# Kernel optimization log

Hardware: AMD Instinct MI355X
Metric: run time of the kernel (lower is better)

## Reference

```python
import jax, jax.numpy as jnp
import numpy as np

THRESHOLD = 0.5
J = 3  # dyadic diffusion scales: collect P^t X at t in {1,2,4,8}
COLLECT = (1, 2, 4, 8)


def setup_inputs() -> dict:
    key = jax.random.key(0)
    k1, k2 = jax.random.split(key)
    B, N, d, n_w = 4, 2048, 32, 4
    point_clouds = jax.random.uniform(k1, (B, N, d), dtype=jnp.float32)
    alphas = jax.random.uniform(k2, (n_w, d), dtype=jnp.float32)
    sigma = jnp.asarray(1.0, dtype=jnp.float32)
    return {"point_clouds": point_clouds, "sigma": sigma, "alphas": alphas}


def reference(point_clouds, sigma, alphas):
    # point_clouds: [B, N, d]; alphas: [Wt, d]
    Xb = point_clouds[:, None, :, :] * alphas[None, :, None, :]  # [B,Wt,N,d]
    # pairwise squared distances (compute_dist): diag(G)+diag(G)^T - 2G
    G = jnp.einsum('bwnd,bwmd->bwnm', Xb, Xb)
    sq = jnp.einsum('bwnd,bwnd->bwn', Xb, Xb)
    D = sq[..., :, None] + sq[..., None, :] - 2.0 * G  # [B,Wt,N,N]
    Wm = jnp.exp(-D / sigma)
    Wm = jnp.where(Wm < THRESHOLD, jnp.zeros_like(Wm), Wm)
    # torch W.sum(0) = column sums; W = W / d is column normalization W[i,j]/d[j]
    col = Wm.sum(axis=-2)  # [B,Wt,N]
    Wn = Wm / col[..., None, :]
    N = Xb.shape[2]
    # edge weights are w/2 plus self-loop edges of weight 0.5 -> lazy walk operator
    P = 0.5 * Wn + 0.5 * jnp.eye(N, dtype=Xb.dtype)
    feats = [Xb]
    x = Xb
    for t in range(1, 2 ** J + 1):
        x = jnp.einsum('bwnm,bwmd->bwnd', P, x)
        if t in COLLECT:
            feats.append(x)
    F = jnp.concatenate(feats, axis=-1)  # [B,Wt,N,(len(COLLECT)+1)*d]
    pooled = F.mean(axis=2)  # global mean pool per graph -> [B,Wt,F]
    B = pooled.shape[0]
    return pooled.reshape(B, -1)  # [B, n_weights * F]
```

## Files before the change

### kernel.cpp

```cpp
#include <hip/hip_runtime.h>


#define NPTS   2048
#define DIM    32
#define BATCH  4
#define NW     4
#define NFEAT  5
#define BLK_PER_B 16
#define NBLK   (BATCH * BLK_PER_B)
#define ROWS   (NPTS / BLK_PER_B)
#define OUT_PER_B (NW * NFEAT * DIM)
#define OUT_TOTAL (BATCH * OUT_PER_B)

__global__ __launch_bounds__(256) void partial_sums(const float* __restrict__ pc,
                                                    float* __restrict__ ws) {
    const int b   = blockIdx.x / BLK_PER_B;
    const int blk = blockIdx.x % BLK_PER_B;
    const int t   = threadIdx.x;

    const float4* base = (const float4*)(pc + (size_t)b * NPTS * DIM
                                            + (size_t)blk * ROWS * DIM);
    float4 s = make_float4(0.f, 0.f, 0.f, 0.f);
#pragma unroll
    for (int i = 0; i < 4; ++i) {
        float4 v = base[t + i * 256];
        s.x += v.x; s.y += v.y; s.z += v.z; s.w += v.w;
    }

    __shared__ float4 sm[256];
    sm[t] = s;
    __syncthreads();
#pragma unroll
    for (int str = 128; str >= 8; str >>= 1) {
        if (t < str) {
            float4 a = sm[t], c = sm[t + str];
            a.x += c.x; a.y += c.y; a.z += c.z; a.w += c.w;
            sm[t] = a;
        }
        __syncthreads();
    }
    if (t < DIM)
        ws[blockIdx.x * DIM + t] = ((const float*)sm)[t];
}

__global__ __launch_bounds__(256) void combine(const float* __restrict__ ws,
                                               const float* __restrict__ alphas,
                                               float* __restrict__ out) {
    const int t = threadIdx.x;
    __shared__ float mean[BATCH * DIM];

    if (t < BATCH * DIM) {
        const int b = t >> 5, j = t & 31;
        float s = 0.f;
#pragma unroll
        for (int k = 0; k < BLK_PER_B; ++k)
            s += ws[(b * BLK_PER_B + k) * DIM + j];
        mean[t] = s * (1.0f / NPTS);
    }
    __syncthreads();

#pragma unroll
    for (int i = 0; i < OUT_TOTAL / 256; ++i) {
        const int idx = t + i * 256;
        const int b = idx / OUT_PER_B;
        const int r = idx % OUT_PER_B;
        const int j = r & 31;
        const int w = r / (NFEAT * DIM);
        out[idx] = mean[b * DIM + j] * alphas[w * DIM + j];
    }
}

extern "C" void kernel_launch(void* const* d_in, const int* in_sizes, int n_in,
                              void* d_out, int out_size, void* d_ws, size_t ws_size,
                              hipStream_t stream) {
    const float* pc     = (const float*)d_in[0];
    const float* alphas = (const float*)d_in[2];
    float*       out    = (float*)d_out;
    float*       ws     = (float*)d_ws;

    partial_sums<<<NBLK, 256, 0, stream>>>(pc, ws);
    combine<<<1, 256, 0, stream>>>(ws, alphas, out);
}
```

Before: 57.88 us.

## Fuse partial-sum and combine kernels into one per-batch block with wave shuffles

Replaces the two-kernel pipeline with a single kernel. One 1024-thread block per batch reduces the point cloud to column means, then writes the alpha-scaled outer-product output directly. Shared-memory tree reductions become wavefront shuffle reductions, and the workspace round-trip is gone. This removes one launch and a global-memory handoff, at the cost of running only 4 blocks, which limits the memory bandwidth available for reading the input.

```diff
diff --git a/kernel.cpp b/kernel.cpp
--- a/kernel.cpp
+++ b/kernel.cpp
@@ -6,67 +6,64 @@
 #define BATCH  4
 #define NW     4
 #define NFEAT  5
-#define BLK_PER_B 16
-#define NBLK   (BATCH * BLK_PER_B)
-#define ROWS   (NPTS / BLK_PER_B)
 #define OUT_PER_B (NW * NFEAT * DIM)
-#define OUT_TOTAL (BATCH * OUT_PER_B)
+#define THREADS   1024
+#define F4_PER_B  (NPTS * DIM / 4)
+#define LOADS     (F4_PER_B / THREADS)
 
-__global__ __launch_bounds__(256) void partial_sums(const float* __restrict__ pc,
-                                                    float* __restrict__ ws) {
-    const int b   = blockIdx.x / BLK_PER_B;
-    const int blk = blockIdx.x % BLK_PER_B;
-    const int t   = threadIdx.x;
+__global__ __launch_bounds__(THREADS) void fused_mean_outer(
+        const float* __restrict__ pc,
+        const float* __restrict__ alphas,
+        float* __restrict__ out) {
+    const int b = blockIdx.x;
+    const int t = threadIdx.x;
 
-    const float4* base = (const float4*)(pc + (size_t)b * NPTS * DIM
-                                            + (size_t)blk * ROWS * DIM);
+    const float4* base = (const float4*)(pc + (size_t)b * NPTS * DIM);
     float4 s = make_float4(0.f, 0.f, 0.f, 0.f);
 #pragma unroll
-    for (int i = 0; i < 4; ++i) {
-        float4 v = base[t + i * 256];
+    for (int i = 0; i < LOADS; ++i) {
+        float4 v = base[t + i * THREADS];
         s.x += v.x; s.y += v.y; s.z += v.z; s.w += v.w;
     }
 
-    __shared__ float4 sm[256];
-    sm[t] = s;
+#pragma unroll
+    for (int off = 8; off < 64; off <<= 1) {
+        s.x += __shfl_xor(s.x, off, 64);
+        s.y += __shfl_xor(s.y, off, 64);
+        s.z += __shfl_xor(s.z, off, 64);
+        s.w += __shfl_xor(s.w, off, 64);
+    }
+
+    __shared__ float4 sm[(THREADS / 64) * 8];
+    __shared__ float  colmean[DIM];
+    const int wave = t >> 6, lane = t & 63;
+    if (lane < 8) sm[wave * 8 + lane] = s;
     __syncthreads();
+
+    if (t < 64) {
+        float4 a = sm[t];
+        float4 c = sm[t + 64];
+        a.x += c.x; a.y += c.y; a.z += c.z; a.w += c.w;
 #pragma unroll
-    for (int str = 128; str >= 8; str >>= 1) {
-        if (t < str) {
-            float4 a = sm[t], c = sm[t + str];
-            a.x += c.x; a.y += c.y; a.z += c.z; a.w += c.w;
-            sm[t] = a;
+        for (int off = 8; off < 64; off <<= 1) {
+            a.x += __shfl_xor(a.x, off, 64);
+            a.y += __shfl_xor(a.y, off, 64);
+            a.z += __shfl_xor(a.z, off, 64);
+            a.w += __shfl_xor(a.w, off, 64);
         }
-        __syncthreads();
-    }
-    if (t < DIM)
-        ws[blockIdx.x * DIM + t] = ((const float*)sm)[t];
-}
-
-__global__ __launch_bounds__(256) void combine(const float* __restrict__ ws,
-                                               const float* __restrict__ alphas,
-                                               float* __restrict__ out) {
-    const int t = threadIdx.x;
-    __shared__ float mean[BATCH * DIM];
-
-    if (t < BATCH * DIM) {
-        const int b = t >> 5, j = t & 31;
-        float s = 0.f;
-#pragma unroll
-        for (int k = 0; k < BLK_PER_B; ++k)
-            s += ws[(b * BLK_PER_B + k) * DIM + j];
-        mean[t] = s * (1.0f / NPTS);
+        if (t < 8) {
+            colmean[t * 4 + 0] = a.x * (1.0f / NPTS);
+            colmean[t * 4 + 1] = a.y * (1.0f / NPTS);
+            colmean[t * 4 + 2] = a.z * (1.0f / NPTS);
+            colmean[t * 4 + 3] = a.w * (1.0f / NPTS);
+        }
     }
     __syncthreads();
 
-#pragma unroll
-    for (int i = 0; i < OUT_TOTAL / 256; ++i) {
-        const int idx = t + i * 256;
-        const int b = idx / OUT_PER_B;
-        const int r = idx % OUT_PER_B;
-        const int j = r & 31;
-        const int w = r / (NFEAT * DIM);
-        out[idx] = mean[b * DIM + j] * alphas[w * DIM + j];
+    if (t < OUT_PER_B) {
+        const int j = t & 31;
+        const int w = t / (NFEAT * DIM);
+        out[b * OUT_PER_B + t] = colmean[j] * alphas[w * DIM + j];
     }
 }
 
@@ -76,8 +73,7 @@
     const float* pc     = (const float*)d_in[0];
     const float* alphas = (const float*)d_in[2];
     float*       out    = (float*)d_out;
-    float*       ws     = (float*)d_ws;
+    (void)d_ws; (void)ws_size;
 
-    partial_sums<<<NBLK, 256, 0, stream>>>(pc, ws);
-    combine<<<1, 256, 0, stream>>>(ws, alphas, out);
+    fused_mean_outer<<<BATCH, THREADS, 0, stream>>>(pc, alphas, out);
 }
```

Result: slower. 59.98 us (+3.6%).
